# Kernel tuning notes

Measured on AMD Instinct MI355X. Metric: run time of the kernel, lower is better.

The kernel has to match this reference:

```python
import jax, jax.numpy as jnp
import numpy as np
import math

D_MODEL = 1024
N_HEADS = 16
HEAD_DIM = D_MODEL // N_HEADS
B, T = 4, 2048


def setup_inputs() -> dict:
    key = jax.random.key(0)
    k1, k2, k3, k4, k5 = jax.random.split(key, 5)
    s = 1.0 / math.sqrt(D_MODEL)
    return {
        "x": jax.random.normal(k1, (B, T, D_MODEL), dtype=jnp.float32),
        "qkv_w": jax.random.normal(k2, (3 * D_MODEL, D_MODEL), dtype=jnp.float32) * s,
        "qkv_b": jax.random.normal(k3, (3 * D_MODEL,), dtype=jnp.float32) * 0.02,
        "out_w": jax.random.normal(k4, (D_MODEL, D_MODEL), dtype=jnp.float32) * s,
        "out_b": jax.random.normal(k5, (D_MODEL,), dtype=jnp.float32) * 0.02,
    }


def reference(x, qkv_w, qkv_b, out_w, out_b) -> jnp.ndarray:
    b, t, c = x.shape
    h, hd = N_HEADS, HEAD_DIM
    # qkv projection: [B,T,3C]
    qkv = jnp.einsum("btc,oc->bto", x, qkv_w) + qkv_b
    qkv = qkv.reshape(b, t, 3, h, hd).transpose(2, 0, 3, 1, 4)  # [3,B,H,T,hd]
    q, k, v = qkv[0], qkv[1], qkv[2]
    scale = 1.0 / math.sqrt(hd)
    attn = jnp.einsum("bhqd,bhkd->bhqk", q, k) * scale  # [B,H,T,T]
    causal = jnp.triu(jnp.ones((t, t), dtype=bool), k=1)
    attn = jnp.where(causal, -jnp.inf, attn)
    attn = jax.nn.softmax(attn, axis=-1)
    out = jnp.einsum("bhqk,bhkd->bhqd", attn, v)  # [B,H,T,hd]
    out = out.transpose(0, 2, 1, 3).reshape(b, t, c)
    return jnp.einsum("btc,oc->bto", out, out_w) + out_b
```

## Files before the change

kernel.cpp:

```cpp
#include <hip/hip_runtime.h>
#include <stdint.h>
#include <stddef.h>

#define TT 2048
#define NH 16
#define HD 64
#define CM 1024
#define QSCALE 0.1803368801f
#define PPAD 72

typedef float f32x4  __attribute__((ext_vector_type(4)));
typedef short bf16x8 __attribute__((ext_vector_type(8)));

static __device__ __forceinline__ unsigned short f32_to_bf16(float f) {
    union { float f; unsigned u; } c; c.f = f;
    unsigned u = c.u;
    u += 0x7FFFu + ((u >> 16) & 1u);
    return (unsigned short)(u >> 16);
}

static __device__ __forceinline__ unsigned pack_bf16_trunc(float lo, float hi) {
    return __builtin_amdgcn_perm(__float_as_uint(hi), __float_as_uint(lo), 0x07060302u);
}

static __device__ __forceinline__ void glds16(const unsigned short* g, unsigned short* l) {
    __builtin_amdgcn_global_load_lds(
        (const __attribute__((address_space(1))) unsigned int*)g,
        (__attribute__((address_space(3))) unsigned int*)l,
        16, 0, 0);
}

static __device__ __forceinline__ void hard_barrier() {
    asm volatile("s_waitcnt vmcnt(0) lgkmcnt(0)" ::: "memory");
    __syncthreads();
}

__global__ __launch_bounds__(256) void cast_all(
    const float* __restrict__ x, const float* __restrict__ w1,
    const float* __restrict__ w2,
    unsigned short* __restrict__ X16, unsigned short* __restrict__ W1o,
    unsigned short* __restrict__ W2o) {
    int i = blockIdx.x * blockDim.x + threadIdx.x;
    const float* src; unsigned short* dst; int j;
    if (i < 2097152)      { src = x;  dst = X16; j = i; }
    else if (i < 2883584) { src = w1; dst = W1o; j = i - 2097152; }
    else                  { src = w2; dst = W2o; j = i - 2883584; }
    float4 v = ((const float4*)src)[j];
    ushort4 o;
    o.x = f32_to_bf16(v.x); o.y = f32_to_bf16(v.y);
    o.z = f32_to_bf16(v.z); o.w = f32_to_bf16(v.w);
    ((ushort4*)dst)[j] = o;
}

template<bool SWAP>
__device__ __forceinline__ void gemm256_core(
    const unsigned short* __restrict__ A,
    const unsigned short* __restrict__ Bm,
    int m0, int n0,
    unsigned short* lds,
    f32x4 acc[8][4])
{
    const int tid  = threadIdx.x;
    const int lane = tid & 63;
    const int w    = tid >> 6;
    const int l15  = lane & 15;
    const int quad = lane >> 4;
    const int wm   = (w >> 1) * 128;
    const int wn   = (w & 1) * 64;
    const int ro   = (quad ^ (l15 & 3)) * 8;

    const int rr = tid >> 2;
    const int ch = (tid & 3) ^ (rr & 3);
    const unsigned short* gA = A  + (size_t)(m0 + rr) * CM + ch * 8;
    const unsigned short* gB = Bm + (size_t)(n0 + rr) * CM + ch * 8;
    const int wb = (tid & ~63) * 8;

    unsigned short* ldsA = lds;
    unsigned short* ldsB = lds + 16384;

#define STAGE6(bb)                                                    \
    {                                                                 \
        unsigned short* dA = ldsA + (bb) * 8192 + wb;                 \
        unsigned short* dB = ldsB + (bb) * 4096 + wb;                 \
        glds16(gA,            dA);                                    \
        glds16(gA +  64 * CM, dA + 2048);                             \
        glds16(gA + 128 * CM, dA + 4096);                             \
        glds16(gA + 192 * CM, dA + 6144);                             \
        glds16(gB,            dB);                                    \
        glds16(gB +  64 * CM, dB + 2048);                             \
        gA += 32; gB += 32;                                           \
    }

    STAGE6(0);
    STAGE6(1);

    for (int t = 0; t < 32; ++t) {
        if (t > 0) {
            asm volatile("s_waitcnt lgkmcnt(0)" ::: "memory");
            __builtin_amdgcn_s_barrier();
            asm volatile("" ::: "memory");
            if (t + 1 < 32) STAGE6((t + 1) & 1);
        }
        if (t + 1 < 32) asm volatile("s_waitcnt vmcnt(6)" ::: "memory");
        else            asm volatile("s_waitcnt vmcnt(0)" ::: "memory");
        __builtin_amdgcn_s_barrier();
        asm volatile("" ::: "memory");

        const unsigned short* tA = ldsA + (t & 1) * 8192;
        const unsigned short* tB = ldsB + (t & 1) * 4096;

        bf16x8 bfr[4];
        #pragma unroll
        for (int ni = 0; ni < 4; ++ni)
            bfr[ni] = *(const bf16x8*)(tB + (wn + ni * 16 + l15) * 32 + ro);
        bf16x8 af[8];
        #pragma unroll
        for (int mi = 0; mi < 8; ++mi)
            af[mi] = *(const bf16x8*)(tA + (wm + mi * 16 + l15) * 32 + ro);

        #pragma unroll
        for (int mi = 0; mi < 8; ++mi)
            #pragma unroll
            for (int ni = 0; ni < 4; ++ni)
                acc[mi][ni] = SWAP
                    ? __builtin_amdgcn_mfma_f32_16x16x32_bf16(bfr[ni], af[mi], acc[mi][ni], 0, 0, 0)
                    : __builtin_amdgcn_mfma_f32_16x16x32_bf16(af[mi], bfr[ni], acc[mi][ni], 0, 0, 0);
    }
#undef STAGE6
}

__global__ __launch_bounds__(256, 2) void gemm_qkv(
    const unsigned short* __restrict__ X,
    const unsigned short* __restrict__ W,
    const float* __restrict__ bias,
    unsigned short* __restrict__ Qb,
    unsigned short* __restrict__ Kb,
    unsigned short* __restrict__ Vt)
{
    __shared__ __align__(16) unsigned short lds[24576];
    const int m0 = blockIdx.y * 256;
    const int n0 = blockIdx.x * 128;

    f32x4 acc[8][4];
    f32x4 z = {0.f, 0.f, 0.f, 0.f};
    #pragma unroll
    for (int mi = 0; mi < 8; ++mi)
        #pragma unroll
        for (int ni = 0; ni < 4; ++ni) acc[mi][ni] = z;

    const int region = n0 >> 10;
    if (region < 2) gemm256_core<true >(X, W, m0, n0, lds, acc);
    else            gemm256_core<false>(X, W, m0, n0, lds, acc);

    const int tid  = threadIdx.x;
    const int lane = tid & 63;
    const int w    = tid >> 6;
    const int wm   = (w >> 1) * 128;
    const int wn   = (w & 1) * 64;
    const int l15  = lane & 15;
    const int quad = lane >> 4;
    const int b_idx = m0 >> 11;
    const int t0 = m0 & 2047;

    if (region == 2) {
        hard_barrier();
        #pragma unroll
        for (int hn = 0; hn < 2; ++hn) {
            if ((w & 1) == hn) {
                #pragma unroll
                for (int ni = 0; ni < 4; ++ni) {
                    const int nloc = ni * 16 + l15;
                    const float bv = bias[n0 + hn * 64 + nloc];
                    #pragma unroll
                    for (int mi = 0; mi < 8; ++mi) {
                        uint2 pk;
                        pk.x = (unsigned)f32_to_bf16(acc[mi][ni][0] + bv) |
                               ((unsigned)f32_to_bf16(acc[mi][ni][1] + bv) << 16);
                        pk.y = (unsigned)f32_to_bf16(acc[mi][ni][2] + bv) |
                               ((unsigned)f32_to_bf16(acc[mi][ni][3] + bv) << 16);
                        *(uint2*)(lds + nloc * 264 + wm + mi * 16 + quad * 4) = pk;
                    }
                }
            }
            hard_barrier();
            {
                const int row = tid >> 2, seg = tid & 3;
                const int o   = n0 + hn * 64 + row;
                const int oin = o & 1023;
                const int hh  = oin >> 6, d = oin & 63;
                unsigned short* dst = Vt + ((size_t)((b_idx << 4) + hh) * HD + d) * TT
                                        + t0 + seg * 64;
                const unsigned short* src = lds + row * 264 + seg * 64;
                #pragma unroll
                for (int u = 0; u < 8; ++u)
                    *(uint4*)(dst + u * 8) = *(const uint4*)(src + u * 8);
            }
            hard_barrier();
        }
        return;
    }

    unsigned short* dst0 = region ? Kb : Qb;
    const float scl = region ? 1.0f : QSCALE;
    #pragma unroll
    for (int mi = 0; mi < 8; ++mi) {
        const int gm = m0 + wm + mi * 16 + l15;
        const int t  = gm & 2047;
        #pragma unroll
        for (int ni = 0; ni < 4; ++ni) {
            const int o  = n0 + wn + ni * 16 + quad * 4;
            const float4 bv = *(const float4*)(bias + o);
            const int oin = o & 1023;
            const int hh = oin >> 6, d = oin & 63;
            const int bh = (b_idx << 4) + hh;
            const float v0 = (acc[mi][ni][0] + bv.x) * scl;
            const float v1 = (acc[mi][ni][1] + bv.y) * scl;
            const float v2 = (acc[mi][ni][2] + bv.z) * scl;
            const float v3 = (acc[mi][ni][3] + bv.w) * scl;
            uint2 pk;
            pk.x = (unsigned)f32_to_bf16(v0) | ((unsigned)f32_to_bf16(v1) << 16);
            pk.y = (unsigned)f32_to_bf16(v2) | ((unsigned)f32_to_bf16(v3) << 16);
            *(uint2*)(dst0 + (((size_t)(bh * TT + t)) << 6) + d) = pk;
        }
    }
}

__global__ __launch_bounds__(256, 2) void attn_kernel(
    const unsigned short* __restrict__ Qb,
    const unsigned short* __restrict__ Kb,
    const unsigned short* __restrict__ Vt,
    unsigned short* __restrict__ CTX)
{
    __shared__ __align__(16) unsigned short Kl[3][4096];
    __shared__ __align__(16) unsigned short Vl[3][4096];
    __shared__ __align__(16) unsigned short Pl[4][16 * PPAD];

    const int id = blockIdx.x;
    const int qt = 15 - (id >> 6);
    const int bh = id & 63;
    const int b  = bh >> 4, h = bh & 15;
    const int tid  = threadIdx.x;
    const int lane = tid & 63;
    const int w    = tid >> 6;
    const int l15  = lane & 15;
    const int quad = lane >> 4;
    const int sw   = l15 & 7;
    const int bhh  = b * NH + h;

    const unsigned short* Kbase = Kb + (size_t)bhh * TT * HD;
    const unsigned short* Vbase = Vt + (size_t)bhh * HD * TT;
    const f32x4 z = {0.f, 0.f, 0.f, 0.f};

    const int c1 = tid, c2 = tid + 256;
    const int row1 = c1 >> 3, col1 = ((c1 & 7) ^ (row1 & 7)) * 8;
    const int row2 = c2 >> 3, col2 = ((c2 & 7) ^ (row2 & 7)) * 8;
    unsigned short* dK1 = &Kl[0][(c1 & ~63) * 8];
    unsigned short* dK2 = &Kl[0][(c2 & ~63) * 8];
    unsigned short* dV1 = &Vl[0][(c1 & ~63) * 8];
    unsigned short* dV2 = &Vl[0][(c2 & ~63) * 8];

    const int len = 2 * qt + 2;
    const int qb0 = qt * 128;

    const unsigned short* kp1 = Kbase + (size_t)row1 * HD + col1;
    const unsigned short* kp2 = Kbase + (size_t)row2 * HD + col2;
    const unsigned short* vp1 = Vbase + (size_t)row1 * TT + col1;
    const unsigned short* vp2 = Vbase + (size_t)row2 * TT + col2;

    bf16x8 qf[2][2];
    #pragma unroll
    for (int f = 0; f < 2; ++f) {
        const unsigned short* qr =
            Qb + (size_t)(bhh * TT + qb0 + f * 64 + w * 16 + l15) * HD + quad * 8;
        qf[f][0] = *(const bf16x8*)(qr);
        qf[f][1] = *(const bf16x8*)(qr + 32);
    }

    f32x4 o_acc[2][4];
    #pragma unroll
    for (int f = 0; f < 2; ++f)
        #pragma unroll
        for (int di = 0; di < 4; ++di) o_acc[f][di] = z;
    float lrun[2] = {0.f, 0.f};

#define STAGE_KV(bufidx)                                               \
    {                                                                  \
        const int nx = (bufidx) * 4096;                                \
        glds16(kp1, dK1 + nx); glds16(kp2, dK2 + nx);                  \
        glds16(vp1, dV1 + nx); glds16(vp2, dV2 + nx);                  \
        kp1 += 64 * HD; kp2 += 64 * HD; vp1 += 64; vp2 += 64;          \
    }
    STAGE_KV(0);
    STAGE_KV(1);
    if (len > 2) STAGE_KV(2);

    for (int i = 0; i < len; ++i) {
        const int cur = i % 3;
        if (i > 0) {
            asm volatile("s_waitcnt lgkmcnt(0)" ::: "memory");
            __builtin_amdgcn_s_barrier();
            asm volatile("" ::: "memory");
            if (i + 2 < len) STAGE_KV((i + 2) % 3);
        }
        if (i + 2 < len)      asm volatile("s_waitcnt vmcnt(8)" ::: "memory");
        else if (i + 1 < len) asm volatile("s_waitcnt vmcnt(4)" ::: "memory");
        else                  asm volatile("s_waitcnt vmcnt(0)" ::: "memory");
        __builtin_amdgcn_s_barrier();
        asm volatile("" ::: "memory");

        const unsigned short* Kt    = &Kl[0][0] + cur * 4096;
        const unsigned short* Vtile = &Vl[0][0] + cur * 4096;
        const bool f0act = (i < len - 1);

        f32x4 s0[4], s1[4];
        #pragma unroll
        for (int ni = 0; ni < 4; ++ni) {
            const unsigned short* kr = Kt + (ni * 16 + l15) * 64;
            bf16x8 kf0 = *(const bf16x8*)(kr + ((quad ^ sw) * 8));
            bf16x8 kf1 = *(const bf16x8*)(kr + (((quad + 4) ^ sw) * 8));
            if (f0act) {
                f32x4 a = __builtin_amdgcn_mfma_f32_16x16x32_bf16(kf0, qf[0][0], z, 0, 0, 0);
                s0[ni] = __builtin_amdgcn_mfma_f32_16x16x32_bf16(kf1, qf[0][1], a, 0, 0, 0);
            }
            f32x4 a1 = __builtin_amdgcn_mfma_f32_16x16x32_bf16(kf0, qf[1][0], z, 0, 0, 0);
            s1[ni] = __builtin_amdgcn_mfma_f32_16x16x32_bf16(kf1, qf[1][1], a1, 0, 0, 0);
        }

        const int qloc = w * 16 + l15;
        if (f0act && i == len - 2) {
            #pragma unroll
            for (int ni = 0; ni < 4; ++ni)
                #pragma unroll
                for (int r = 0; r < 4; ++r)
                    if (ni * 16 + quad * 4 + r > qloc) s0[ni][r] = -1e30f;
        }
        if (i == len - 1) {
            #pragma unroll
            for (int ni = 0; ni < 4; ++ni)
                #pragma unroll
                for (int r = 0; r < 4; ++r)
                    if (ni * 16 + quad * 4 + r > qloc) s1[ni][r] = -1e30f;
        }

        #define SOFTMAX_P(S, F)                                              \
        {                                                                    \
            float tni[4];                                                    \
            _Pragma("unroll")                                                \
            for (int ni = 0; ni < 4; ++ni) {                                 \
                float p0 = __builtin_amdgcn_exp2f(S[ni][0]);                 \
                float p1 = __builtin_amdgcn_exp2f(S[ni][1]);                 \
                float p2 = __builtin_amdgcn_exp2f(S[ni][2]);                 \
                float p3 = __builtin_amdgcn_exp2f(S[ni][3]);                 \
                S[ni][0] = p0; S[ni][1] = p1; S[ni][2] = p2; S[ni][3] = p3;  \
                tni[ni] = (p0 + p1) + (p2 + p3);                             \
            }                                                                \
            lrun[F] += (tni[0] + tni[1]) + (tni[2] + tni[3]);                \
            unsigned short* pwf = Pl[w];                                     \
            _Pragma("unroll")                                                \
            for (int ni = 0; ni < 4; ++ni) {                                 \
                uint2 pk;                                                    \
                pk.x = pack_bf16_trunc(S[ni][0], S[ni][1]);                  \
                pk.y = pack_bf16_trunc(S[ni][2], S[ni][3]);                  \
                *(uint2*)(pwf + l15 * PPAD + ni * 16 + quad * 4) = pk;       \
            }                                                                \
        }

        bf16x8 vf[2][4];
        SOFTMAX_P(s1, 1);
        asm volatile("s_waitcnt lgkmcnt(0)" ::: "memory");
        #pragma unroll
        for (int c = 0; c < 2; ++c) {
            bf16x8 pf1 = *(const bf16x8*)(Pl[w] + l15 * PPAD + c * 32 + quad * 8);
            #pragma unroll
            for (int di = 0; di < 4; ++di) {
                vf[c][di] = *(const bf16x8*)(Vtile + (di * 16 + l15) * 64
                                           + (((c * 4 + quad) ^ sw) * 8));
                o_acc[1][di] = __builtin_amdgcn_mfma_f32_16x16x32_bf16(vf[c][di], pf1, o_acc[1][di], 0, 0, 0);
            }
        }
        if (f0act) {
            SOFTMAX_P(s0, 0);
            asm volatile("s_waitcnt lgkmcnt(0)" ::: "memory");
            #pragma unroll
            for (int c = 0; c < 2; ++c) {
                bf16x8 pf0 = *(const bf16x8*)(Pl[w] + l15 * PPAD + c * 32 + quad * 8);
                #pragma unroll
                for (int di = 0; di < 4; ++di)
                    o_acc[0][di] = __builtin_amdgcn_mfma_f32_16x16x32_bf16(vf[c][di], pf0, o_acc[0][di], 0, 0, 0);
            }
        }
        #undef SOFTMAX_P
    }
#undef STAGE_KV

    #pragma unroll
    for (int f = 0; f < 2; ++f) {
        float lt = lrun[f];
        lt += __shfl_xor(lt, 16);
        lt += __shfl_xor(lt, 32);
        const float inv = 1.0f / lt;
        unsigned short* crow =
            CTX + (size_t)(b * TT + qb0 + f * 64 + w * 16 + l15) * CM + h * HD;
        #pragma unroll
        for (int di = 0; di < 4; ++di) {
            uint2 pk;
            pk.x = (unsigned)f32_to_bf16(o_acc[f][di][0] * inv) |
                   ((unsigned)f32_to_bf16(o_acc[f][di][1] * inv) << 16);
            pk.y = (unsigned)f32_to_bf16(o_acc[f][di][2] * inv) |
                   ((unsigned)f32_to_bf16(o_acc[f][di][3] * inv) << 16);
            *(uint2*)(crow + di * 16 + quad * 4) = pk;
        }
    }
}

__global__ __launch_bounds__(256, 2) void gemm_out(
    const unsigned short* __restrict__ CTX,
    const unsigned short* __restrict__ W,
    const float* __restrict__ bias,
    float* __restrict__ out)
{
    __shared__ __align__(16) unsigned short lds[24576];
    const int m0 = blockIdx.y * 256;
    const int n0 = blockIdx.x * 128;

    f32x4 acc[8][4];
    f32x4 z = {0.f, 0.f, 0.f, 0.f};
    #pragma unroll
    for (int mi = 0; mi < 8; ++mi)
        #pragma unroll
        for (int ni = 0; ni < 4; ++ni) acc[mi][ni] = z;

    gemm256_core<true>(CTX, W, m0, n0, lds, acc);

    const int tid  = threadIdx.x;
    const int lane = tid & 63;
    const int w    = tid >> 6;
    const int wm   = (w >> 1) * 128;
    const int wn   = (w & 1) * 64;
    const int l15  = lane & 15;
    const int quad = lane >> 4;

    #pragma unroll
    for (int mi = 0; mi < 8; ++mi) {
        const int gm = m0 + wm + mi * 16 + l15;
        float* orow = out + (size_t)gm * CM;
        #pragma unroll
        for (int ni = 0; ni < 4; ++ni) {
            const int o = n0 + wn + ni * 16 + quad * 4;
            const float4 bv = *(const float4*)(bias + o);
            float4 v;
            v.x = acc[mi][ni][0] + bv.x;
            v.y = acc[mi][ni][1] + bv.y;
            v.z = acc[mi][ni][2] + bv.z;
            v.w = acc[mi][ni][3] + bv.w;
            *(float4*)(orow + o) = v;
        }
    }
}

extern "C" void kernel_launch(void* const* d_in, const int* in_sizes, int n_in,
                              void* d_out, int out_size, void* d_ws, size_t ws_size,
                              hipStream_t stream) {
    const float* x     = (const float*)d_in[0];
    const float* qkv_w = (const float*)d_in[1];
    const float* qkv_b = (const float*)d_in[2];
    const float* out_w = (const float*)d_in[3];
    const float* out_b = (const float*)d_in[4];
    float* out = (float*)d_out;

    char* ws = (char*)d_ws;
    unsigned short* X16 = (unsigned short*)(ws + 0);
    unsigned short* W1  = (unsigned short*)(ws + 16777216);
    unsigned short* W2  = (unsigned short*)(ws + 23068672);
    unsigned short* Qb  = (unsigned short*)(ws + 25165824);
    unsigned short* Kb  = (unsigned short*)(ws + 41943040);
    unsigned short* Vt  = (unsigned short*)(ws + 58720256);
    unsigned short* CTX = (unsigned short*)(ws + 75497472);

    cast_all<<<12288, 256, 0, stream>>>(x, qkv_w, out_w, X16, W1, W2);

    gemm_qkv<<<dim3(24, 32), 256, 0, stream>>>(X16, W1, qkv_b, Qb, Kb, Vt);
    attn_kernel<<<1024, 256, 0, stream>>>(Qb, Kb, Vt, CTX);
    gemm_out<<<dim3(8, 32), 256, 0, stream>>>(CTX, W2, out_b, out);
}
```

Before: 262.0 us.

## Replace LDS P staging with bpermute shuffles, double-buffer KV, remap blocks to XCDs

The attention kernel no longer writes softmax probabilities to shared memory and reads them back. It rearranges the packed bf16 P fragments across lanes with ds_bpermute so they form the MFMA operand layout directly. KV staging drops from triple to double buffering, which shrinks LDS so launch bounds can allow 3 blocks per CU. Block indices are also remapped so the heads of a batch cluster on the same XCD for L2 locality. The cost is more bpermute instructions, higher register pressure under the tighter bound, and one less stage of prefetch depth to hide load latency.

```diff
diff --git a/kernel.cpp b/kernel.cpp
--- a/kernel.cpp
+++ b/kernel.cpp
@@ -7,7 +7,6 @@
 #define HD 64
 #define CM 1024
 #define QSCALE 0.1803368801f
-#define PPAD 72
 
 typedef float f32x4  __attribute__((ext_vector_type(4)));
 typedef short bf16x8 __attribute__((ext_vector_type(8)));
@@ -225,19 +224,19 @@
     }
 }
 
-__global__ __launch_bounds__(256, 2) void attn_kernel(
+__global__ __launch_bounds__(256, 3) void attn_kernel(
     const unsigned short* __restrict__ Qb,
     const unsigned short* __restrict__ Kb,
     const unsigned short* __restrict__ Vt,
     unsigned short* __restrict__ CTX)
 {
-    __shared__ __align__(16) unsigned short Kl[3][4096];
-    __shared__ __align__(16) unsigned short Vl[3][4096];
-    __shared__ __align__(16) unsigned short Pl[4][16 * PPAD];
-
-    const int id = blockIdx.x;
-    const int qt = 15 - (id >> 6);
-    const int bh = id & 63;
+    __shared__ __align__(16) unsigned short Kl[2][4096];
+    __shared__ __align__(16) unsigned short Vl[2][4096];
+
+    const int id  = blockIdx.x;
+    const int xcd = id & 7, j = id >> 3;
+    const int bh  = (xcd << 3) | (j & 7);
+    const int qt  = 15 - (j >> 3);
     const int b  = bh >> 4, h = bh & 15;
     const int tid  = threadIdx.x;
     const int lane = tid & 63;
@@ -283,6 +282,10 @@
         for (int di = 0; di < 4; ++di) o_acc[f][di] = z;
     float lrun[2] = {0.f, 0.f};
 
+    const int srcA = (l15 + 32 * (quad & 1)) * 4;
+    const int srcB = srcA + 64;
+    const bool selhi = (quad >> 1) != 0;
+
 #define STAGE_KV(bufidx)                                               \
     {                                                                  \
         const int nx = (bufidx) * 4096;                                \
@@ -291,20 +294,18 @@
         kp1 += 64 * HD; kp2 += 64 * HD; vp1 += 64; vp2 += 64;          \
     }
     STAGE_KV(0);
-    STAGE_KV(1);
-    if (len > 2) STAGE_KV(2);
+    if (len > 1) STAGE_KV(1);
 
     for (int i = 0; i < len; ++i) {
-        const int cur = i % 3;
+        const int cur = i & 1;
         if (i > 0) {
             asm volatile("s_waitcnt lgkmcnt(0)" ::: "memory");
             __builtin_amdgcn_s_barrier();
             asm volatile("" ::: "memory");
-            if (i + 2 < len) STAGE_KV((i + 2) % 3);
-        }
-        if (i + 2 < len)      asm volatile("s_waitcnt vmcnt(8)" ::: "memory");
-        else if (i + 1 < len) asm volatile("s_waitcnt vmcnt(4)" ::: "memory");
-        else                  asm volatile("s_waitcnt vmcnt(0)" ::: "memory");
+            if (i + 1 < len) STAGE_KV((i + 1) & 1);
+        }
+        if (i + 1 < len) asm volatile("s_waitcnt vmcnt(4)" ::: "memory");
+        else             asm volatile("s_waitcnt vmcnt(0)" ::: "memory");
         __builtin_amdgcn_s_barrier();
         asm volatile("" ::: "memory");
 
@@ -342,54 +343,58 @@
                     if (ni * 16 + quad * 4 + r > qloc) s1[ni][r] = -1e30f;
         }
 
-        #define SOFTMAX_P(S, F)                                              \
+        bf16x8 pf0[2], pf1[2];
+        #define SOFTMAX_X(S, PF, F)                                          \
         {                                                                    \
             float tni[4];                                                    \
+            unsigned pkA[4], pkB[4];                                         \
             _Pragma("unroll")                                                \
             for (int ni = 0; ni < 4; ++ni) {                                 \
                 float p0 = __builtin_amdgcn_exp2f(S[ni][0]);                 \
                 float p1 = __builtin_amdgcn_exp2f(S[ni][1]);                 \
                 float p2 = __builtin_amdgcn_exp2f(S[ni][2]);                 \
                 float p3 = __builtin_amdgcn_exp2f(S[ni][3]);                 \
-                S[ni][0] = p0; S[ni][1] = p1; S[ni][2] = p2; S[ni][3] = p3;  \
                 tni[ni] = (p0 + p1) + (p2 + p3);                             \
+                pkA[ni] = pack_bf16_trunc(p0, p1);                           \
+                pkB[ni] = pack_bf16_trunc(p2, p3);                           \
             }                                                                \
             lrun[F] += (tni[0] + tni[1]) + (tni[2] + tni[3]);                \
-            unsigned short* pwf = Pl[w];                                     \
             _Pragma("unroll")                                                \
-            for (int ni = 0; ni < 4; ++ni) {                                 \
-                uint2 pk;                                                    \
-                pk.x = pack_bf16_trunc(S[ni][0], S[ni][1]);                  \
-                pk.y = pack_bf16_trunc(S[ni][2], S[ni][3]);                  \
-                *(uint2*)(pwf + l15 * PPAD + ni * 16 + quad * 4) = pk;       \
+            for (int c = 0; c < 2; ++c) {                                    \
+                const int n0i = 2 * c, n1i = 2 * c + 1;                      \
+                unsigned q00 = __builtin_amdgcn_ds_bpermute(srcA, pkA[n0i]); \
+                unsigned q01 = __builtin_amdgcn_ds_bpermute(srcA, pkB[n0i]); \
+                unsigned q02 = __builtin_amdgcn_ds_bpermute(srcB, pkA[n0i]); \
+                unsigned q03 = __builtin_amdgcn_ds_bpermute(srcB, pkB[n0i]); \
+                unsigned q10 = __builtin_amdgcn_ds_bpermute(srcA, pkA[n1i]); \
+                unsigned q11 = __builtin_amdgcn_ds_bpermute(srcA, pkB[n1i]); \
+                unsigned q12 = __builtin_amdgcn_ds_bpermute(srcB, pkA[n1i]); \
+                unsigned q13 = __builtin_amdgcn_ds_bpermute(srcB, pkB[n1i]); \
+                union { unsigned u[4]; bf16x8 v8; } uu;                      \
+                uu.u[0] = selhi ? q10 : q00;                                 \
+                uu.u[1] = selhi ? q11 : q01;                                 \
+                uu.u[2] = selhi ? q12 : q02;                                 \
+                uu.u[3] = selhi ? q13 : q03;                                 \
+                PF[c] = uu.v8;                                               \
             }                                                                \
         }
 
-        bf16x8 vf[2][4];
-        SOFTMAX_P(s1, 1);
-        asm volatile("s_waitcnt lgkmcnt(0)" ::: "memory");
+        SOFTMAX_X(s1, pf1, 1);
+        if (f0act) SOFTMAX_X(s0, pf0, 0);
+        #undef SOFTMAX_X
+
         #pragma unroll
         for (int c = 0; c < 2; ++c) {
-            bf16x8 pf1 = *(const bf16x8*)(Pl[w] + l15 * PPAD + c * 32 + quad * 8);
             #pragma unroll
             for (int di = 0; di < 4; ++di) {
-                vf[c][di] = *(const bf16x8*)(Vtile + (di * 16 + l15) * 64
-                                           + (((c * 4 + quad) ^ sw) * 8));
-                o_acc[1][di] = __builtin_amdgcn_mfma_f32_16x16x32_bf16(vf[c][di], pf1, o_acc[1][di], 0, 0, 0);
+                const unsigned short* vr = Vtile + (di * 16 + l15) * 64
+                                         + (((c * 4 + quad) ^ sw) * 8);
+                bf16x8 vf = *(const bf16x8*)(vr);
+                o_acc[1][di] = __builtin_amdgcn_mfma_f32_16x16x32_bf16(vf, pf1[c], o_acc[1][di], 0, 0, 0);
+                if (f0act)
+                    o_acc[0][di] = __builtin_amdgcn_mfma_f32_16x16x32_bf16(vf, pf0[c], o_acc[0][di], 0, 0, 0);
             }
         }
-        if (f0act) {
-            SOFTMAX_P(s0, 0);
-            asm volatile("s_waitcnt lgkmcnt(0)" ::: "memory");
-            #pragma unroll
-            for (int c = 0; c < 2; ++c) {
-                bf16x8 pf0 = *(const bf16x8*)(Pl[w] + l15 * PPAD + c * 32 + quad * 8);
-                #pragma unroll
-                for (int di = 0; di < 4; ++di)
-                    o_acc[0][di] = __builtin_amdgcn_mfma_f32_16x16x32_bf16(vf[c][di], pf0, o_acc[0][di], 0, 0, 0);
-            }
-        }
-        #undef SOFTMAX_P
     }
 #undef STAGE_KV
 
```

New measurement: 456.0 us. 1.74x slower.
